# Optimization experiments

Measured on AMD Instinct MI355X. Metric: run time of the kernel, lower is better.

Reference implementation:

```python
import jax, jax.numpy as jnp
import numpy as np

N, F, H, K = 4096, 512, 256, 8
NEG = -1e9


def _attention(h, mask, a_w, a_b):
    # h: [N,H]; mask: [N,N] bool; a_w: [K,2H]; a_b: [K]
    # per-head logits[i,j] = lrelu(a_src . h_i + a_dst . h_j + b), softmax over
    # neighbors j (A[i,j]==1); out_i = h_i + sum_j alpha_ij h_j; isolated nodes
    # (no neighbors) keep h_i unchanged (alpha row masked to zero).
    Hd = h.shape[1]
    src = h @ a_w[:, :Hd].T + a_b[None, :]   # [N,K]
    dst = h @ a_w[:, Hd:].T                  # [N,K]
    fmask = mask.astype(h.dtype)
    outs = []
    for k in range(a_w.shape[0]):
        logits = jax.nn.leaky_relu(src[:, k][:, None] + dst[:, k][None, :], 0.01)
        logits = jnp.where(mask, logits, NEG)
        alpha = jax.nn.softmax(logits, axis=1) * fmask  # zero rows for isolated nodes
        outs.append(h + alpha @ h)
    return outs


def setup_inputs() -> dict:
    key = jax.random.key(0)
    ks = jax.random.split(key, 12)
    s = 0.02
    adjacency = jax.random.randint(ks[0], (N, N), 0, 2).astype(jnp.float32)
    feats = jax.random.normal(ks[1], (N, F), dtype=jnp.float32)
    return {
        "adjacency": adjacency,
        "feats": feats,
        "W1_w": jax.random.normal(ks[2], (H, F), dtype=jnp.float32) * s,
        "W1_b": jnp.zeros((H,), jnp.float32),
        "a1_w": jax.random.normal(ks[3], (K, 2 * H), dtype=jnp.float32) * s,
        "a1_b": jnp.zeros((K,), jnp.float32),
        "W2_w": jax.random.normal(ks[4], (H, K * H), dtype=jnp.float32) * s,
        "W2_b": jnp.zeros((H,), jnp.float32),
        "a2_w": jax.random.normal(ks[5], (K, 2 * H), dtype=jnp.float32) * s,
        "a2_b": jnp.zeros((K,), jnp.float32),
        "out_w": jax.random.normal(ks[6], (1, H), dtype=jnp.float32) * s,
        "out_b": jnp.zeros((1,), jnp.float32),
    }


def reference(adjacency, feats, W1_w, W1_b, a1_w, a1_b, W2_w, W2_b, a2_w, a2_b, out_w, out_b):
    mask = adjacency == 1.0
    # torch.inner(A, feats.T) == A @ feats; dropout is identity in eval mode
    h1 = (adjacency @ feats) @ W1_w.T + W1_b            # [N,H]
    heads1 = _attention(h1, mask, a1_w, a1_b)           # K x [N,H]
    h1_new = jax.nn.elu(jnp.concatenate(heads1, axis=1))  # [N,K*H]
    h2 = h1_new @ W2_w.T + W2_b                         # [N,H]
    heads2 = _attention(h2, mask, a2_w, a2_b)
    avg = sum(heads2) / a2_w.shape[0]                   # [N,H]
    h2_new = jax.nn.elu(avg)
    avgd = jnp.mean(h2_new, axis=0)                     # [H]
    return avgd @ out_w.T + out_b                       # [1]
```

## Files before the change

kernel.cpp:

```cpp
#include <hip/hip_runtime.h>
#include <hip/hip_bf16.h>
#include <hip/hip_fp16.h>


#define NN 4096
#define FF 512
#define HH 256
#define KK 8
#define KH 2048

typedef __attribute__((ext_vector_type(8))) short bf16x8;
typedef __attribute__((ext_vector_type(4))) float f32x4;
typedef __attribute__((ext_vector_type(16))) float f32x16;
typedef _Float16 h16x2 __attribute__((ext_vector_type(2)));
typedef _Float16 h16x8 __attribute__((ext_vector_type(8)));

__device__ inline short f2bf(float x) {
    __hip_bfloat16 b = __float2bfloat16(x);
    return *reinterpret_cast<short*>(&b);
}
__device__ inline short to_bf(float x) { return f2bf(x); }
__device__ inline short to_bf(short x) { return x; }

__device__ inline unsigned int pkh(float a, float b) {
    auto r = __builtin_amdgcn_cvt_pkrtz(a, b);
    unsigned int u;
    __builtin_memcpy(&u, &r, 4);
    return u;
}
__device__ inline unsigned int h2mul(unsigned int a, unsigned int b) {
    h16x2 av, bv;
    __builtin_memcpy(&av, &a, 4);
    __builtin_memcpy(&bv, &b, 4);
    h16x2 r = av * bv;
    unsigned int u;
    __builtin_memcpy(&u, &r, 4);
    return u;
}
__device__ inline unsigned int h2max(unsigned int a, unsigned int b) {
    h16x2 av, bv;
    __builtin_memcpy(&av, &a, 4);
    __builtin_memcpy(&bv, &b, 4);
    h16x2 r = __builtin_elementwise_max(av, bv);
    unsigned int u;
    __builtin_memcpy(&u, &r, 4);
    return u;
}
__device__ inline float h2dot1(unsigned int a, float c) {
    h16x2 av;
    __builtin_memcpy(&av, &a, 4);
    h16x2 one = {(_Float16)1.0f, (_Float16)1.0f};
    return __builtin_amdgcn_fdot2(av, one, c, false);
}

__device__ inline unsigned int enc_f(float x) {
    unsigned int u = __float_as_uint(x);
    return (u & 0x80000000u) ? ~u : (u | 0x80000000u);
}
__device__ inline float dec_f(unsigned int e) {
    unsigned int u = (e & 0x80000000u) ? (e ^ 0x80000000u) : ~e;
    return __uint_as_float(u);
}

__global__ void pack_mask_kernel(const float* __restrict__ adj,
                                 unsigned int* __restrict__ mbits) {
    int i = blockIdx.x;
    int lane = threadIdx.x & 63;
    int wv = threadIdx.x >> 6;
    for (int j0 = wv * 64; j0 < NN; j0 += 256) {
        float v = adj[(size_t)i * NN + j0 + lane];
        unsigned long long b = __ballot(v == 1.0f);
        if (lane == 0) {
            mbits[i * 128 + (j0 >> 5)]     = (unsigned int)(b & 0xffffffffull);
            mbits[i * 128 + (j0 >> 5) + 1] = (unsigned int)(b >> 32);
        }
    }
}

template <typename T>
__global__ __launch_bounds__(256) void cvt_a_frag_kernel(const T* __restrict__ src,
                                                         bf16x8* __restrict__ dst, int K) {
    int t = threadIdx.x, lane = t & 63, w = t >> 6, mt = blockIdx.x;
    int Kt = K >> 5;
    int m = mt * 16 + (lane & 15), kq = (lane >> 4) * 8;
    for (int kt = w; kt < Kt; kt += 4) {
        size_t base = (size_t)m * K + kt * 32 + kq;
        bf16x8 v;
#pragma unroll
        for (int jj = 0; jj < 8; jj++) v[jj] = to_bf(src[base + jj]);
        dst[((size_t)mt * Kt + kt) * 64 + lane] = v;
    }
}

__global__ __launch_bounds__(256) void cvt_bt2_kernel(const float* __restrict__ W1,
                                                      const float* __restrict__ W2,
                                                      bf16x8* __restrict__ d1,
                                                      bf16x8* __restrict__ d2) {
    const float* Wm = blockIdx.y ? W2 : W1;
    bf16x8* dst = blockIdx.y ? d2 : d1;
    int K = blockIdx.y ? KH : FF;
    constexpr int Nt = HH / 16;
    int t = threadIdx.x, lane = t & 63, w = t >> 6, nt = blockIdx.x;
    int Kt = K >> 5;
    int n = nt * 16 + (lane & 15), kq = (lane >> 4) * 8;
    for (int kt = w; kt < Kt; kt += 4) {
        size_t base = (size_t)n * K + kt * 32 + kq;
        bf16x8 v;
#pragma unroll
        for (int jj = 0; jj < 8; jj++) v[jj] = f2bf(Wm[base + jj]);
        dst[((size_t)kt * Nt + nt) * 64 + lane] = v;
    }
}

template <int W>
__global__ __launch_bounds__(256) void cvt_b_frag_kernel(const float* __restrict__ src,
                                                         bf16x8* __restrict__ dst) {
    __shared__ float hs[32][W + 8];
    constexpr int Nt = W / 16;
    int t = threadIdx.x, jb = blockIdx.x;
    {
        int r = t >> 3, cb = (t & 7) * (W / 8);
        const float* sp = &src[(size_t)(jb * 32 + r) * W + cb];
#pragma unroll
        for (int q = 0; q < W / 32; q++) *(float4*)&hs[r][cb + q * 4] = *(const float4*)&sp[q * 4];
    }
    __syncthreads();
    for (int id = t; id < Nt * 64; id += 256) {
        int nt = id >> 6, lane = id & 63;
        int c = nt * 16 + (lane & 15), q8 = (lane >> 4) * 8;
        bf16x8 v;
#pragma unroll
        for (int jj = 0; jj < 8; jj++) v[jj] = f2bf(hs[q8 + jj][c]);
        dst[((size_t)jb * Nt + nt) * 64 + lane] = v;
    }
}

__global__ __launch_bounds__(256) void gemm_frag_kernel(
    const bf16x8* __restrict__ Af, const bf16x8* __restrict__ Bf,
    const float* __restrict__ bias, float* __restrict__ C,
    int Kt, int Nt, int Nrow) {
    int t = threadIdx.x, lane = t & 63, w = t >> 6;
    int quad = lane >> 4, c16 = lane & 15;
    int wm = w & 1, wn = w >> 1;
    int mt0 = blockIdx.y * 4 + wm * 2;
    int nt0 = blockIdx.x * 4 + wn * 2;
    f32x4 acc[2][2];
#pragma unroll
    for (int i = 0; i < 2; i++)
#pragma unroll
        for (int j = 0; j < 2; j++) acc[i][j] = (f32x4){0.f, 0.f, 0.f, 0.f};
    const bf16x8* ap = Af + (size_t)mt0 * Kt * 64 + lane;
    const bf16x8* bp = Bf + (size_t)nt0 * 64 + lane;
#pragma unroll 4
    for (int kt = 0; kt < Kt; kt++) {
        bf16x8 a0 = ap[(size_t)kt * 64];
        bf16x8 a1 = ap[((size_t)Kt + kt) * 64];
        bf16x8 b0 = bp[(size_t)kt * Nt * 64];
        bf16x8 b1 = bp[((size_t)kt * Nt + 1) * 64];
        acc[0][0] = __builtin_amdgcn_mfma_f32_16x16x32_bf16(a0, b0, acc[0][0], 0, 0, 0);
        acc[0][1] = __builtin_amdgcn_mfma_f32_16x16x32_bf16(a0, b1, acc[0][1], 0, 0, 0);
        acc[1][0] = __builtin_amdgcn_mfma_f32_16x16x32_bf16(a1, b0, acc[1][0], 0, 0, 0);
        acc[1][1] = __builtin_amdgcn_mfma_f32_16x16x32_bf16(a1, b1, acc[1][1], 0, 0, 0);
    }
#pragma unroll
    for (int i = 0; i < 2; i++) {
#pragma unroll
        for (int j = 0; j < 2; j++) {
            int n = (nt0 + j) * 16 + c16;
            float bv = bias ? bias[n] : 0.f;
#pragma unroll
            for (int reg = 0; reg < 4; reg++) {
                int m = (mt0 + i) * 16 + quad * 4 + reg;
                C[(size_t)m * Nrow + n] = acc[i][j][reg] + bv;
            }
        }
    }
}

__global__ __launch_bounds__(256) void gemm_adj_kernel(
    const unsigned int* __restrict__ mbits, const bf16x8* __restrict__ Bf,
    float* __restrict__ C, int Kt, int Nt, int Nrow) {
    int t = threadIdx.x, lane = t & 63, w = t >> 6;
    int quad = lane >> 4, c16 = lane & 15;
    int wm = w & 1, wn = w >> 1;
    int mt = blockIdx.y * 2 + wm;
    int nt0 = blockIdx.x * 8 + wn * 4;
    int row = mt * 16 + (lane & 15), q8 = (lane >> 4) * 8;
    f32x4 acc[4];
#pragma unroll
    for (int j = 0; j < 4; j++) acc[j] = (f32x4){0.f, 0.f, 0.f, 0.f};
    const bf16x8* bp = Bf + (size_t)nt0 * 64 + lane;
#pragma unroll 2
    for (int kt = 0; kt < Kt; kt++) {
        unsigned int w0 = mbits[(size_t)row * 128 + kt];
        unsigned int mb0 = (w0 >> q8) & 0xffu;
        union { unsigned int u[4]; bf16x8 v; } A0;
#pragma unroll
        for (int jp = 0; jp < 4; jp++) {
            unsigned int u0 = (mb0 >> (2 * jp)) & 3u;
            A0.u[jp] = ((u0 * 0x8001u) & 0x10001u) * 0x3F80u;
        }
        bf16x8 b0 = bp[(size_t)kt * Nt * 64];
        bf16x8 b1 = bp[((size_t)kt * Nt + 1) * 64];
        bf16x8 b2 = bp[((size_t)kt * Nt + 2) * 64];
        bf16x8 b3 = bp[((size_t)kt * Nt + 3) * 64];
        acc[0] = __builtin_amdgcn_mfma_f32_16x16x32_bf16(A0.v, b0, acc[0], 0, 0, 0);
        acc[1] = __builtin_amdgcn_mfma_f32_16x16x32_bf16(A0.v, b1, acc[1], 0, 0, 0);
        acc[2] = __builtin_amdgcn_mfma_f32_16x16x32_bf16(A0.v, b2, acc[2], 0, 0, 0);
        acc[3] = __builtin_amdgcn_mfma_f32_16x16x32_bf16(A0.v, b3, acc[3], 0, 0, 0);
    }
#pragma unroll
    for (int j = 0; j < 4; j++) {
        int n = (nt0 + j) * 16 + c16;
#pragma unroll
        for (int reg = 0; reg < 4; reg++) {
            int mm = mt * 16 + quad * 4 + reg;
            C[(size_t)mm * Nrow + n] = acc[j][reg];
        }
    }
}

__global__ __launch_bounds__(256) void prep_kernel(const float* __restrict__ h,
                                                   const float* __restrict__ aw,
                                                   const float* __restrict__ ab,
                                                   h16x8* __restrict__ HB16,
                                                   float* __restrict__ srcT,
                                                   float* __restrict__ dstT,
                                                   unsigned int* __restrict__ maxd_u) {
    __shared__ __align__(16) float hs[32][264];
    __shared__ __align__(16) float awl[KK * 512];
    int t = threadIdx.x, jb = blockIdx.x;
#pragma unroll
    for (int q = 0; q < 4; q++)
        *(float4*)&awl[(t + q * 256) * 4] = *(const float4*)&aw[(t + q * 256) * 4];
    {
        int r = t >> 3, cb = (t & 7) * 32;
        const float* hp = &h[(size_t)(jb * 32 + r) * HH + cb];
#pragma unroll
        for (int q = 0; q < 8; q++) *(float4*)&hs[r][cb + q * 4] = *(const float4*)&hp[q * 4];
    }
    __syncthreads();
#pragma unroll
    for (int it = 0; it < 4; it++) {
        int id = t + it * 256;
        int q = id >> 9, nt = (id >> 6) & 7, lane = id & 63;
        int c = nt * 32 + (lane & 31), j8 = q * 16 + (lane >> 5) * 8;
        union { unsigned int u[4]; h16x8 v; } pk;
#pragma unroll
        for (int jp = 0; jp < 4; jp++)
            pk.u[jp] = pkh(hs[j8 + 2 * jp][c], hs[j8 + 2 * jp + 1][c]);
        HB16[((size_t)(jb * 2 + q)) * 512 + nt * 64 + lane] = pk.v;
    }
    {
        const float LOG2E = 1.4426950408889634f;
        int row = t & 31, head = t >> 5;
        float s = ab[head], d = 0.f;
        const float* ws = &awl[head * 512];
        const float* wd = ws + 256;
#pragma unroll 4
        for (int c = 0; c < 256; c += 4) {
            float4 hv = *(const float4*)&hs[row][c];
            float4 a4 = *(const float4*)&ws[c];
            float4 b4 = *(const float4*)&wd[c];
            s += hv.x * a4.x + hv.y * a4.y + hv.z * a4.z + hv.w * a4.w;
            d += hv.x * b4.x + hv.y * b4.y + hv.z * b4.z + hv.w * b4.w;
        }
        float ds = d * LOG2E;
        srcT[head * NN + jb * 32 + row] = s * LOG2E;
        dstT[head * NN + jb * 32 + row] = ds;
        float mx = ds;
#pragma unroll
        for (int off = 16; off > 0; off >>= 1) mx = fmaxf(mx, __shfl_xor(mx, off));
        if (row == 0) atomicMax(&maxd_u[head], enc_f(mx));
    }
}

template <int MODE>
__global__ __launch_bounds__(256, 2) void attn32_kernel(
    const float* __restrict__ h, const float* __restrict__ srcT,
    const float* __restrict__ dstT, const unsigned int* __restrict__ maxd_u,
    const unsigned int* __restrict__ mbits, const h16x8* __restrict__ HB16,
    void* __restrict__ outp) {
    __shared__ __align__(16) char smraw[49600];
    __shared__ float l_all[2][2][32];
    __shared__ float linv_l[2][32];
    unsigned short* e1t = (unsigned short*)smraw;
    unsigned short* e2t = (unsigned short*)(smraw + 16384);
    unsigned int* mrow = (unsigned int*)(smraw + 32768);
    float* accbuf = (float*)smraw;

    int t = threadIdx.x;
    int i0 = blockIdx.x * 32;
    int k0 = blockIdx.y * 2;

    float Dv0 = dec_f(maxd_u[k0]), Dv1 = dec_f(maxd_u[k0 + 1]);
#pragma unroll
    for (int q = 0; q < 8; q++) {
        int idx = t + q * 256;
        int hh = idx >> 10, off = (idx & 1023) * 4;
        float D = hh ? Dv1 : Dv0;
        float4 dv = *(const float4*)&dstT[(size_t)(k0 + hh) * NN + off];
        float d0 = dv.x - D, d1 = dv.y - D, d2 = dv.z - D, d3 = dv.w - D;
        uint2 p1, p2;
        p1.x = pkh(__builtin_amdgcn_exp2f(d0), __builtin_amdgcn_exp2f(d1));
        p1.y = pkh(__builtin_amdgcn_exp2f(d2), __builtin_amdgcn_exp2f(d3));
        p2.x = pkh(__builtin_amdgcn_exp2f(0.01f * d0), __builtin_amdgcn_exp2f(0.01f * d1));
        p2.y = pkh(__builtin_amdgcn_exp2f(0.01f * d2), __builtin_amdgcn_exp2f(0.01f * d3));
        *(uint2*)&e1t[hh * 4096 + off] = p1;
        *(uint2*)&e2t[hh * 4096 + off] = p2;
    }
#pragma unroll
    for (int q = 0; q < 16; q++) {
        int idx = t + q * 256;
        int r = idx >> 7, wd = idx & 127;
        mrow[r * 131 + wd] = mbits[(size_t)(i0 + r) * 128 + wd];
    }
    __syncthreads();

    int lane = t & 63, w = t >> 6;
    int jh = w & 1, ch = w >> 1;
    int rowl = lane & 31, jsub = (lane >> 5) * 8;

    unsigned int AcPk[2], BcPk[2];
    float lacc[2] = {0.f, 0.f};
#pragma unroll
    for (int hh = 0; hh < 2; hh++) {
        float sL = srcT[(size_t)(k0 + hh) * NN + i0 + rowl];
        float xm = sL + (hh ? Dv1 : Dv0);
        float mL = fmaxf(xm, 0.01f * xm);
        float Acf = __builtin_amdgcn_exp2f(xm - mL);
        float Bcf = __builtin_amdgcn_exp2f(fmaf(0.01f, xm, -mL));
        AcPk[hh] = pkh(Acf, Acf);
        BcPk[hh] = pkh(Bcf, Bcf);
    }

    f32x16 acc[2][4];
#pragma unroll
    for (int hh = 0; hh < 2; hh++)
#pragma unroll
        for (int nt = 0; nt < 4; nt++)
#pragma unroll
            for (int r = 0; r < 16; r++) acc[hh][nt][r] = 0.f;

    const unsigned short* e1b0 = e1t;
    const unsigned short* e1b1 = e1t + 4096;
    const unsigned short* e2b0 = e2t;
    const unsigned short* e2b1 = e2t + 4096;

    int jbase = jh * 128;
    const h16x8* bpbase = HB16 + (size_t)(ch * 4) * 64 + lane;
    h16x8 bv0, bv1, bv2, bv3;
    {
        const h16x8* bp = bpbase + (size_t)jbase * 512;
        bv0 = bp[0]; bv1 = bp[64]; bv2 = bp[128]; bv3 = bp[192];
    }

#pragma unroll 2
    for (int it = 0; it < 128; it++) {
        int j16 = jbase + it;
        h16x8 nb0, nb1, nb2, nb3;
        {
            const h16x8* bp = bpbase + (size_t)(j16 + 1) * 512;
            nb0 = bp[0]; nb1 = bp[64]; nb2 = bp[128]; nb3 = bp[192];
        }
        unsigned int word = mrow[rowl * 131 + (j16 >> 1)];
        unsigned int mb = (word >> ((j16 & 1) * 16 + jsub)) & 0xffu;
        unsigned int mw[4];
#pragma unroll
        for (int jp = 0; jp < 4; jp++) {
            unsigned int u2 = (mb >> (2 * jp)) & 3u;
            mw[jp] = ((u2 * 0x8001u) & 0x10001u) * 0xffffu;
        }
        int eoff = j16 * 16 + jsub;
        union { unsigned int u[4]; h16x8 v; } P0;
        {
            uint4 E1 = *(const uint4*)&e1b0[eoff];
            uint4 E2 = *(const uint4*)&e2b0[eoff];
            unsigned int v0 = h2max(h2mul(E1.x, AcPk[0]), h2mul(E2.x, BcPk[0])) & mw[0];
            unsigned int v1 = h2max(h2mul(E1.y, AcPk[0]), h2mul(E2.y, BcPk[0])) & mw[1];
            unsigned int v2 = h2max(h2mul(E1.z, AcPk[0]), h2mul(E2.z, BcPk[0])) & mw[2];
            unsigned int v3 = h2max(h2mul(E1.w, AcPk[0]), h2mul(E2.w, BcPk[0])) & mw[3];
            lacc[0] = h2dot1(v0, lacc[0]);
            lacc[0] = h2dot1(v1, lacc[0]);
            lacc[0] = h2dot1(v2, lacc[0]);
            lacc[0] = h2dot1(v3, lacc[0]);
            P0.u[0] = v0; P0.u[1] = v1; P0.u[2] = v2; P0.u[3] = v3;
        }
        acc[0][0] = __builtin_amdgcn_mfma_f32_32x32x16_f16(P0.v, bv0, acc[0][0], 0, 0, 0);
        acc[0][1] = __builtin_amdgcn_mfma_f32_32x32x16_f16(P0.v, bv1, acc[0][1], 0, 0, 0);
        acc[0][2] = __builtin_amdgcn_mfma_f32_32x32x16_f16(P0.v, bv2, acc[0][2], 0, 0, 0);
        acc[0][3] = __builtin_amdgcn_mfma_f32_32x32x16_f16(P0.v, bv3, acc[0][3], 0, 0, 0);
        union { unsigned int u[4]; h16x8 v; } P1;
        {
            uint4 E1 = *(const uint4*)&e1b1[eoff];
            uint4 E2 = *(const uint4*)&e2b1[eoff];
            unsigned int v0 = h2max(h2mul(E1.x, AcPk[1]), h2mul(E2.x, BcPk[1])) & mw[0];
            unsigned int v1 = h2max(h2mul(E1.y, AcPk[1]), h2mul(E2.y, BcPk[1])) & mw[1];
            unsigned int v2 = h2max(h2mul(E1.z, AcPk[1]), h2mul(E2.z, BcPk[1])) & mw[2];
            unsigned int v3 = h2max(h2mul(E1.w, AcPk[1]), h2mul(E2.w, BcPk[1])) & mw[3];
            lacc[1] = h2dot1(v0, lacc[1]);
            lacc[1] = h2dot1(v1, lacc[1]);
            lacc[1] = h2dot1(v2, lacc[1]);
            lacc[1] = h2dot1(v3, lacc[1]);
            P1.u[0] = v0; P1.u[1] = v1; P1.u[2] = v2; P1.u[3] = v3;
        }
        acc[1][0] = __builtin_amdgcn_mfma_f32_32x32x16_f16(P1.v, bv0, acc[1][0], 0, 0, 0);
        acc[1][1] = __builtin_amdgcn_mfma_f32_32x32x16_f16(P1.v, bv1, acc[1][1], 0, 0, 0);
        acc[1][2] = __builtin_amdgcn_mfma_f32_32x32x16_f16(P1.v, bv2, acc[1][2], 0, 0, 0);
        acc[1][3] = __builtin_amdgcn_mfma_f32_32x32x16_f16(P1.v, bv3, acc[1][3], 0, 0, 0);
        bv0 = nb0; bv1 = nb1; bv2 = nb2; bv3 = nb3;
    }

    lacc[0] += __shfl_xor(lacc[0], 32);
    lacc[1] += __shfl_xor(lacc[1], 32);
    if (ch == 0 && lane < 32) {
        l_all[jh][0][lane] = lacc[0];
        l_all[jh][1][lane] = lacc[1];
    }
    __syncthreads();
    if (t < 32) {
#pragma unroll
        for (int hh = 0; hh < 2; hh++) {
            float lt = l_all[0][hh][t] + l_all[1][hh][t];
            linv_l[hh][t] = (lt > 0.f) ? 1.f / lt : 0.f;
        }
    }
    __syncthreads();

#pragma unroll
    for (int r = 0; r < 2; r++) {
        if (jh == 1) {
#pragma unroll
            for (int nt = 0; nt < 4; nt++) {
                float* dp = accbuf + (size_t)((ch * 4 + nt) * 16) * 64 + lane;
#pragma unroll
                for (int reg = 0; reg < 16; reg++) dp[reg * 64] = acc[r][nt][reg];
            }
        }
        __syncthreads();
        if (jh == 0) {
            int khead = k0 + r;
#pragma unroll
            for (int nt = 0; nt < 4; nt++) {
                const float* sp = accbuf + (size_t)((ch * 4 + nt) * 16) * 64 + lane;
                int c = (ch * 4 + nt) * 32 + (lane & 31);
#pragma unroll
                for (int reg = 0; reg < 16; reg++) {
                    int rowloc = (reg & 3) + 8 * (reg >> 2) + 4 * (lane >> 5);
                    float v = (acc[r][nt][reg] + sp[reg * 64]) * linv_l[r][rowloc];
                    int i = i0 + rowloc;
                    if (MODE == 1) {
                        v += h[(size_t)i * HH + c];
                        v = (v > 0.f) ? v : (__expf(v) - 1.f);
                        ((short*)outp)[(size_t)i * KH + (size_t)khead * HH + c] = f2bf(v);
                    } else {
                        ((short*)outp)[(size_t)khead * NN * HH + (size_t)i * HH + c] = f2bf(v);
                    }
                }
            }
        }
        if (r == 0) __syncthreads();
    }
}

__global__ void colsum_kernel(const float* __restrict__ h2,
                              const short* __restrict__ heads,
                              float* __restrict__ partial) {
    int c = threadIdx.x;
    int b = blockIdx.x;
    float s = 0.f;
    for (int il = 0; il < 16; il++) {
        int i = b * 16 + il;
        float v = h2[(size_t)i * HH + c];
#pragma unroll
        for (int k = 0; k < KK; k++) {
            unsigned int bits = (unsigned int)(unsigned short)heads[(size_t)k * NN * HH + (size_t)i * HH + c];
            v += 0.125f * __uint_as_float(bits << 16);
        }
        s += (v > 0.f) ? v : (__expf(v) - 1.f);
    }
    partial[b * HH + c] = s;
}

__global__ void final_kernel(const float* __restrict__ partial,
                             const float* __restrict__ out_w,
                             const float* __restrict__ out_b,
                             float* __restrict__ dout) {
    __shared__ float red[256];
    int c = threadIdx.x;
    float s = 0.f;
    for (int b = 0; b < 256; b++) s += partial[b * HH + c];
    red[c] = (s / 4096.f) * out_w[c];
    __syncthreads();
    for (int off = 128; off > 0; off >>= 1) {
        if (c < off) red[c] += red[c + off];
        __syncthreads();
    }
    if (c == 0) dout[0] = red[0] + out_b[0];
}

extern "C" void kernel_launch(void* const* d_in, const int* in_sizes, int n_in,
                              void* d_out, int out_size, void* d_ws, size_t ws_size,
                              hipStream_t stream) {
    (void)in_sizes; (void)n_in; (void)out_size; (void)ws_size;
    const float* adj   = (const float*)d_in[0];
    const float* feats = (const float*)d_in[1];
    const float* W1_w  = (const float*)d_in[2];
    const float* W1_b  = (const float*)d_in[3];
    const float* a1_w  = (const float*)d_in[4];
    const float* a1_b  = (const float*)d_in[5];
    const float* W2_w  = (const float*)d_in[6];
    const float* W2_b  = (const float*)d_in[7];
    const float* a2_w  = (const float*)d_in[8];
    const float* a2_b  = (const float*)d_in[9];
    const float* out_w = (const float*)d_in[10];
    const float* out_b = (const float*)d_in[11];

    char* w = (char*)d_ws;
    const size_t MB = 1ull << 20;
    const size_t KB = 1ull << 10;
    unsigned int* mbits = (unsigned int*)(w);
    bf16x8* Bfeats = (bf16x8*)(w + 2 * MB);
    float*  tmp1   = (float*)(w + 6 * MB);
    bf16x8* tmp1a  = (bf16x8*)(w + 14 * MB);
    short*  h1nb   = (short*)(w + 2 * MB);
    short*  planes = (short*)(w + 2 * MB);
    bf16x8* h1na   = (bf16x8*)(w + 18 * MB);
    float*  h2     = (float*)(w + 34 * MB);
    float*  h1     = (float*)(w + 38 * MB);
    h16x8*  HB16   = (h16x8*)(w + 42 * MB);
    bf16x8* W1f    = (bf16x8*)(w + 44 * MB);
    bf16x8* W2f    = (bf16x8*)(w + 44 * MB + 256 * KB);
    float*  srcT   = (float*)(w + 45 * MB + 256 * KB);
    float*  dstT   = (float*)(w + 45 * MB + 384 * KB);
    unsigned int* maxd_u = (unsigned int*)(w + 45 * MB + 512 * KB);
    float*  partial = (float*)(w + 45 * MB + 768 * KB);

    pack_mask_kernel<<<NN, 256, 0, stream>>>(adj, mbits);
    cvt_b_frag_kernel<FF><<<NN / 32, 256, 0, stream>>>(feats, Bfeats);
    cvt_bt2_kernel<<<dim3(HH / 16, 2), 256, 0, stream>>>(W1_w, W2_w, W1f, W2f);
    gemm_adj_kernel<<<dim3(FF / 128, NN / 32), 256, 0, stream>>>(
        mbits, Bfeats, tmp1, NN / 32, FF / 16, FF);
    cvt_a_frag_kernel<float><<<NN / 16, 256, 0, stream>>>(tmp1, tmp1a, FF);
    gemm_frag_kernel<<<dim3(HH / 64, NN / 64), 256, 0, stream>>>(
        tmp1a, W1f, W1_b, h1, FF / 32, HH / 16, HH);

    (void)hipMemsetAsync(maxd_u, 0, KK * sizeof(unsigned int), stream);
    prep_kernel<<<NN / 32, 256, 0, stream>>>(h1, a1_w, a1_b, HB16, srcT, dstT, maxd_u);
    attn32_kernel<1><<<dim3(NN / 32, KK / 2), 256, 0, stream>>>(
        h1, srcT, dstT, maxd_u, mbits, HB16, h1nb);
    cvt_a_frag_kernel<short><<<NN / 16, 256, 0, stream>>>(h1nb, h1na, KH);
    gemm_frag_kernel<<<dim3(HH / 64, NN / 64), 256, 0, stream>>>(
        h1na, W2f, W2_b, h2, KH / 32, HH / 16, HH);

    (void)hipMemsetAsync(maxd_u, 0, KK * sizeof(unsigned int), stream);
    prep_kernel<<<NN / 32, 256, 0, stream>>>(h2, a2_w, a2_b, HB16, srcT, dstT, maxd_u);
    attn32_kernel<2><<<dim3(NN / 32, KK / 2), 256, 0, stream>>>(
        h2, srcT, dstT, maxd_u, mbits, HB16, planes);
    colsum_kernel<<<256, 256, 0, stream>>>(h2, planes, partial);
    final_kernel<<<1, 256, 0, stream>>>(partial, out_w, out_b, (float*)d_out);
}
```

Measured before the change: 450.7 us.

## Fuse MFMA fragment packing into GEMM and attention epilogues, drop memsets

The adjacency GEMM and the layer-1 attention epilogue now stage bf16 results in shared memory and write them straight out in the MFMA A-fragment layout. This removes the two separate cvt_a_frag passes and the fp32 intermediate buffer. The two hipMemsetAsync calls are replaced by zeroing both max buffers inside pack_mask_kernel, using separate slots per layer. In exchange the kernels gain extra LDS traffic and a block sync, and attention shared memory grows slightly.

```diff
diff --git a/kernel.cpp b/kernel.cpp
--- a/kernel.cpp
+++ b/kernel.cpp
@@ -19,8 +19,6 @@
     __hip_bfloat16 b = __float2bfloat16(x);
     return *reinterpret_cast<short*>(&b);
 }
-__device__ inline short to_bf(float x) { return f2bf(x); }
-__device__ inline short to_bf(short x) { return x; }
 
 __device__ inline unsigned int pkh(float a, float b) {
     auto r = __builtin_amdgcn_cvt_pkrtz(a, b);
@@ -63,8 +61,10 @@
 }
 
 __global__ void pack_mask_kernel(const float* __restrict__ adj,
-                                 unsigned int* __restrict__ mbits) {
+                                 unsigned int* __restrict__ mbits,
+                                 unsigned int* __restrict__ maxd_u) {
     int i = blockIdx.x;
+    if (i == 0 && threadIdx.x < 16) maxd_u[threadIdx.x] = 0;
     int lane = threadIdx.x & 63;
     int wv = threadIdx.x >> 6;
     for (int j0 = wv * 64; j0 < NN; j0 += 256) {
@@ -74,21 +74,6 @@
             mbits[i * 128 + (j0 >> 5)]     = (unsigned int)(b & 0xffffffffull);
             mbits[i * 128 + (j0 >> 5) + 1] = (unsigned int)(b >> 32);
         }
-    }
-}
-
-template <typename T>
-__global__ __launch_bounds__(256) void cvt_a_frag_kernel(const T* __restrict__ src,
-                                                         bf16x8* __restrict__ dst, int K) {
-    int t = threadIdx.x, lane = t & 63, w = t >> 6, mt = blockIdx.x;
-    int Kt = K >> 5;
-    int m = mt * 16 + (lane & 15), kq = (lane >> 4) * 8;
-    for (int kt = w; kt < Kt; kt += 4) {
-        size_t base = (size_t)m * K + kt * 32 + kq;
-        bf16x8 v;
-#pragma unroll
-        for (int jj = 0; jj < 8; jj++) v[jj] = to_bf(src[base + jj]);
-        dst[((size_t)mt * Kt + kt) * 64 + lane] = v;
     }
 }
 
@@ -179,7 +164,8 @@
 
 __global__ __launch_bounds__(256) void gemm_adj_kernel(
     const unsigned int* __restrict__ mbits, const bf16x8* __restrict__ Bf,
-    float* __restrict__ C, int Kt, int Nt, int Nrow) {
+    bf16x8* __restrict__ Afrag, int Kt, int Nt) {
+    __shared__ unsigned short otA[32][136];
     int t = threadIdx.x, lane = t & 63, w = t >> 6;
     int quad = lane >> 4, c16 = lane & 15;
     int wm = w & 1, wn = w >> 1;
@@ -210,13 +196,18 @@
         acc[3] = __builtin_amdgcn_mfma_f32_16x16x32_bf16(A0.v, b3, acc[3], 0, 0, 0);
     }
 #pragma unroll
-    for (int j = 0; j < 4; j++) {
-        int n = (nt0 + j) * 16 + c16;
-#pragma unroll
-        for (int reg = 0; reg < 4; reg++) {
-            int mm = mt * 16 + quad * 4 + reg;
-            C[(size_t)mm * Nrow + n] = acc[j][reg];
-        }
+    for (int j = 0; j < 4; j++)
+#pragma unroll
+        for (int reg = 0; reg < 4; reg++)
+            otA[wm * 16 + quad * 4 + reg][(wn * 4 + j) * 16 + c16] = (unsigned short)f2bf(acc[j][reg]);
+    __syncthreads();
+#pragma unroll
+    for (int q = 0; q < 2; q++) {
+        int idx = t + q * 256;
+        int mtl = idx >> 8, ktl = (idx >> 6) & 3, lane2 = idx & 63;
+        int r2 = mtl * 16 + (lane2 & 15), colb = ktl * 32 + (lane2 >> 4) * 8;
+        bf16x8 v = *(bf16x8*)&otA[r2][colb];
+        Afrag[((size_t)(blockIdx.y * 2 + mtl) * 16 + (blockIdx.x * 4 + ktl)) * 64 + lane2] = v;
     }
 }
 
@@ -281,13 +272,14 @@
     const float* __restrict__ dstT, const unsigned int* __restrict__ maxd_u,
     const unsigned int* __restrict__ mbits, const h16x8* __restrict__ HB16,
     void* __restrict__ outp) {
-    __shared__ __align__(16) char smraw[49600];
+    __shared__ __align__(16) char smraw[49664];
     __shared__ float l_all[2][2][32];
     __shared__ float linv_l[2][32];
     unsigned short* e1t = (unsigned short*)smraw;
     unsigned short* e2t = (unsigned short*)(smraw + 16384);
     unsigned int* mrow = (unsigned int*)(smraw + 32768);
     float* accbuf = (float*)smraw;
+    unsigned short* ot = (unsigned short*)(smraw + 32768);
 
     int t = threadIdx.x;
     int i0 = blockIdx.x * 32;
@@ -429,6 +421,7 @@
 
 #pragma unroll
     for (int r = 0; r < 2; r++) {
+        int khead = k0 + r;
         if (jh == 1) {
 #pragma unroll
             for (int nt = 0; nt < 4; nt++) {
@@ -438,28 +431,49 @@
             }
         }
         __syncthreads();
-        if (jh == 0) {
-            int khead = k0 + r;
-#pragma unroll
-            for (int nt = 0; nt < 4; nt++) {
-                const float* sp = accbuf + (size_t)((ch * 4 + nt) * 16) * 64 + lane;
-                int c = (ch * 4 + nt) * 32 + (lane & 31);
-#pragma unroll
-                for (int reg = 0; reg < 16; reg++) {
-                    int rowloc = (reg & 3) + 8 * (reg >> 2) + 4 * (lane >> 5);
-                    float v = (acc[r][nt][reg] + sp[reg * 64]) * linv_l[r][rowloc];
-                    int i = i0 + rowloc;
-                    if (MODE == 1) {
-                        v += h[(size_t)i * HH + c];
+        if (MODE == 1) {
+            if (jh == 0) {
+#pragma unroll
+                for (int nt = 0; nt < 4; nt++) {
+                    const float* sp = accbuf + (size_t)((ch * 4 + nt) * 16) * 64 + lane;
+                    int c = (ch * 4 + nt) * 32 + (lane & 31);
+#pragma unroll
+                    for (int reg = 0; reg < 16; reg++) {
+                        int rowloc = (reg & 3) + 8 * (reg >> 2) + 4 * (lane >> 5);
+                        float v = (acc[r][nt][reg] + sp[reg * 64]) * linv_l[r][rowloc];
+                        v += h[(size_t)(i0 + rowloc) * HH + c];
                         v = (v > 0.f) ? v : (__expf(v) - 1.f);
-                        ((short*)outp)[(size_t)i * KH + (size_t)khead * HH + c] = f2bf(v);
-                    } else {
-                        ((short*)outp)[(size_t)khead * NN * HH + (size_t)i * HH + c] = f2bf(v);
+                        ot[rowloc * 264 + c] = (unsigned short)f2bf(v);
                     }
                 }
             }
-        }
-        if (r == 0) __syncthreads();
+            __syncthreads();
+            bf16x8* dstf = (bf16x8*)outp;
+#pragma unroll
+            for (int q = 0; q < 4; q++) {
+                int idx = t + q * 256;
+                int mtl = idx >> 9, ktl = (idx >> 6) & 7, lane2 = idx & 63;
+                int r2 = mtl * 16 + (lane2 & 15), colb = ktl * 32 + (lane2 >> 4) * 8;
+                bf16x8 v = *(bf16x8*)&ot[r2 * 264 + colb];
+                dstf[((size_t)(blockIdx.x * 2 + mtl) * 64 + (khead * 8 + ktl)) * 64 + lane2] = v;
+            }
+            if (r == 0) __syncthreads();
+        } else {
+            if (jh == 0) {
+#pragma unroll
+                for (int nt = 0; nt < 4; nt++) {
+                    const float* sp = accbuf + (size_t)((ch * 4 + nt) * 16) * 64 + lane;
+                    int c = (ch * 4 + nt) * 32 + (lane & 31);
+#pragma unroll
+                    for (int reg = 0; reg < 16; reg++) {
+                        int rowloc = (reg & 3) + 8 * (reg >> 2) + 4 * (lane >> 5);
+                        float v = (acc[r][nt][reg] + sp[reg * 64]) * linv_l[r][rowloc];
+                        ((short*)outp)[(size_t)khead * NN * HH + (size_t)(i0 + rowloc) * HH + c] = f2bf(v);
+                    }
+                }
+            }
+            if (r == 0) __syncthreads();
+        }
     }
 }
 
@@ -521,9 +535,7 @@
     const size_t KB = 1ull << 10;
     unsigned int* mbits = (unsigned int*)(w);
     bf16x8* Bfeats = (bf16x8*)(w + 2 * MB);
-    float*  tmp1   = (float*)(w + 6 * MB);
     bf16x8* tmp1a  = (bf16x8*)(w + 14 * MB);
-    short*  h1nb   = (short*)(w + 2 * MB);
     short*  planes = (short*)(w + 2 * MB);
     bf16x8* h1na   = (bf16x8*)(w + 18 * MB);
     float*  h2     = (float*)(w + 34 * MB);
@@ -536,27 +548,23 @@
     unsigned int* maxd_u = (unsigned int*)(w + 45 * MB + 512 * KB);
     float*  partial = (float*)(w + 45 * MB + 768 * KB);
 
-    pack_mask_kernel<<<NN, 256, 0, stream>>>(adj, mbits);
+    pack_mask_kernel<<<NN, 256, 0, stream>>>(adj, mbits, maxd_u);
     cvt_b_frag_kernel<FF><<<NN / 32, 256, 0, stream>>>(feats, Bfeats);
     cvt_bt2_kernel<<<dim3(HH / 16, 2), 256, 0, stream>>>(W1_w, W2_w, W1f, W2f);
     gemm_adj_kernel<<<dim3(FF / 128, NN / 32), 256, 0, stream>>>(
-        mbits, Bfeats, tmp1, NN / 32, FF / 16, FF);
-    cvt_a_frag_kernel<float><<<NN / 16, 256, 0, stream>>>(tmp1, tmp1a, FF);
+        mbits, Bfeats, tmp1a, NN / 32, FF / 16);
     gemm_frag_kernel<<<dim3(HH / 64, NN / 64), 256, 0, stream>>>(
         tmp1a, W1f, W1_b, h1, FF / 32, HH / 16, HH);
 
-    (void)hipMemsetAsync(maxd_u, 0, KK * sizeof(unsigned int), stream);
     prep_kernel<<<NN / 32, 256, 0, stream>>>(h1, a1_w, a1_b, HB16, srcT, dstT, maxd_u);
     attn32_kernel<1><<<dim3(NN / 32, KK / 2), 256, 0, stream>>>(
-        h1, srcT, dstT, maxd_u, mbits, HB16, h1nb);
-    cvt_a_frag_kernel<short><<<NN / 16, 256, 0, stream>>>(h1nb, h1na, KH);
+        h1, srcT, dstT, maxd_u, mbits, HB16, h1na);
     gemm_frag_kernel<<<dim3(HH / 64, NN / 64), 256, 0, stream>>>(
         h1na, W2f, W2_b, h2, KH / 32, HH / 16, HH);
 
-    (void)hipMemsetAsync(maxd_u, 0, KK * sizeof(unsigned int), stream);
-    prep_kernel<<<NN / 32, 256, 0, stream>>>(h2, a2_w, a2_b, HB16, srcT, dstT, maxd_u);
+    prep_kernel<<<NN / 32, 256, 0, stream>>>(h2, a2_w, a2_b, HB16, srcT, dstT, maxd_u + 8);
     attn32_kernel<2><<<dim3(NN / 32, KK / 2), 256, 0, stream>>>(
-        h2, srcT, dstT, maxd_u, mbits, HB16, planes);
+        h2, srcT, dstT, maxd_u + 8, mbits, HB16, planes);
     colsum_kernel<<<256, 256, 0, stream>>>(h2, planes, partial);
     final_kernel<<<1, 256, 0, stream>>>(partial, out_w, out_b, (float*)d_out);
 }
```

After: 424.8 us. 1.06x faster.
